# Optimization experiments

Measured on AMD Instinct MI355X. Metric: run time of the kernel, lower is better.

## Reference

```python
import jax, jax.numpy as jnp
import numpy as np

HIDDEN = 1024
HEADS = 16
HEAD_DIM = HIDDEN // HEADS


def setup_inputs() -> dict:
    key = jax.random.key(0)
    ks = jax.random.split(key, 11)
    s = 1.0 / np.sqrt(HIDDEN)
    return {
        "query": jax.random.normal(ks[0], (8, 1024, HIDDEN), dtype=jnp.float32),
        "key": jax.random.normal(ks[1], (8, 1024, HIDDEN), dtype=jnp.float32),
        "value": jax.random.normal(ks[2], (8, 1024, HIDDEN), dtype=jnp.float32),
        "Wq": jax.random.uniform(ks[3], (HIDDEN, HIDDEN), jnp.float32, -s, s),
        "bq": jax.random.uniform(ks[4], (HIDDEN,), jnp.float32, -s, s),
        "Wk": jax.random.uniform(ks[5], (HIDDEN, HIDDEN), jnp.float32, -s, s),
        "bk": jax.random.uniform(ks[6], (HIDDEN,), jnp.float32, -s, s),
        "Wv": jax.random.uniform(ks[7], (HIDDEN, HIDDEN), jnp.float32, -s, s),
        "bv": jax.random.uniform(ks[8], (HIDDEN,), jnp.float32, -s, s),
        "Wo": jax.random.uniform(ks[9], (HIDDEN, HIDDEN), jnp.float32, -s, s),
        "bo": jax.random.uniform(ks[10], (HIDDEN,), jnp.float32, -s, s),
    }


def reference(query, key, value, Wq, bq, Wk, bk, Wv, bv, Wo, bo):
    B, S, D = key.shape
    scale = jnp.sqrt(jnp.asarray(HEAD_DIM, dtype=query.dtype))
    # linear projections (torch Linear: x @ W.T + b), split into heads -> [B,H,S,hd]
    def proj(x, W, b):
        return (x @ W.T + b).reshape(B, -1, HEADS, HEAD_DIM).transpose(0, 2, 1, 3)
    q = proj(query, Wq, bq)
    k = proj(key, Wk, bk)
    v = proj(value, Wv, bv)
    # [B,H,Sq,Sk] full attention scores (module materializes them)
    energy = jnp.einsum("bhqd,bhkd->bhqk", q, k) / scale
    attention = jax.nn.softmax(energy, axis=-1)
    # dropout p=0.0 -> identity
    x = jnp.einsum("bhqk,bhkd->bhqd", attention, v)
    x = x.transpose(0, 2, 1, 3).reshape(B, -1, D)
    return x @ Wo.T + bo
```

## Files before the change

kernel.cpp:

```cpp
#include <hip/hip_runtime.h>
#include <hip/hip_bf16.h>
#include <stdint.h>

#define HIDDEN 1024
#define HEADS 16
#define HD 64
#define BATCH 8
#define SEQ 1024
#define MTOT (BATCH*SEQ)

typedef __attribute__((ext_vector_type(4))) float  f32x4;
typedef __attribute__((ext_vector_type(4))) float  float4v;
typedef __attribute__((ext_vector_type(8))) short  s16x8;
typedef __attribute__((ext_vector_type(4))) short  s16x4;
typedef __attribute__((ext_vector_type(4))) unsigned int u32x4;
typedef __bf16 bf16x8 __attribute__((ext_vector_type(8)));

#define QSCALE 0.18033688011112042f

__device__ __forceinline__ short f2bf(float f) {
  uint32_t u = __builtin_bit_cast(uint32_t, f);
  u += 0x7FFFu + ((u >> 16) & 1u);
  return (short)(u >> 16);
}
__device__ __forceinline__ bf16x8 asbf(s16x8 v) {
  return __builtin_bit_cast(bf16x8, v);
}

__device__ __forceinline__ float dpp_fmax16(float x) {
  int t;
  t = __builtin_amdgcn_update_dpp(0, __builtin_bit_cast(int, x), 0xB1, 0xF, 0xF, true);
  x = fmaxf(x, __builtin_bit_cast(float, t));
  t = __builtin_amdgcn_update_dpp(0, __builtin_bit_cast(int, x), 0x4E, 0xF, 0xF, true);
  x = fmaxf(x, __builtin_bit_cast(float, t));
  t = __builtin_amdgcn_update_dpp(0, __builtin_bit_cast(int, x), 0x141, 0xF, 0xF, true);
  x = fmaxf(x, __builtin_bit_cast(float, t));
  t = __builtin_amdgcn_update_dpp(0, __builtin_bit_cast(int, x), 0x140, 0xF, 0xF, true);
  x = fmaxf(x, __builtin_bit_cast(float, t));
  return x;
}
__device__ __forceinline__ float dpp_fadd16(float x) {
  int t;
  t = __builtin_amdgcn_update_dpp(0, __builtin_bit_cast(int, x), 0xB1, 0xF, 0xF, true);
  x += __builtin_bit_cast(float, t);
  t = __builtin_amdgcn_update_dpp(0, __builtin_bit_cast(int, x), 0x4E, 0xF, 0xF, true);
  x += __builtin_bit_cast(float, t);
  t = __builtin_amdgcn_update_dpp(0, __builtin_bit_cast(int, x), 0x141, 0xF, 0xF, true);
  x += __builtin_bit_cast(float, t);
  t = __builtin_amdgcn_update_dpp(0, __builtin_bit_cast(int, x), 0x140, 0xF, 0xF, true);
  x += __builtin_bit_cast(float, t);
  return x;
}

typedef const __attribute__((address_space(1))) void* gvp;
typedef __attribute__((address_space(3)))       void* lvp;
__device__ __forceinline__ void gl_lds16(const void* g, const void* ldsbase) {
  __builtin_amdgcn_global_load_lds((gvp)(uintptr_t)g,
                                   (lvp)(uintptr_t)(uint32_t)(uintptr_t)ldsbase,
                                   16, 0, 0);
}

__global__ __launch_bounds__(256) void cvt_x(const float* __restrict__ src,
                                             short* __restrict__ dst) {
  int i = blockIdx.x * 256 + threadIdx.x;
  float4v a = *(const float4v*)(src + (size_t)i * 8);
  float4v b = *(const float4v*)(src + (size_t)i * 8 + 4);
  s16x8 o = { f2bf(a.x), f2bf(a.y), f2bf(a.z), f2bf(a.w),
              f2bf(b.x), f2bf(b.y), f2bf(b.z), f2bf(b.w) };
  *(s16x8*)(dst + (size_t)i * 8) = o;
}

__global__ __launch_bounds__(256) void cvt_w(const float* __restrict__ s0,
                                             const float* __restrict__ s1,
                                             const float* __restrict__ s2,
                                             const float* __restrict__ s3,
                                             short* __restrict__ dst) {
  int z = blockIdx.y;
  const float* src = (z == 0) ? s0 : (z == 1) ? s1 : (z == 2) ? s2 : s3;
  int i = blockIdx.x * 256 + threadIdx.x;
  float4v a = *(const float4v*)(src + (size_t)i * 8);
  float4v b = *(const float4v*)(src + (size_t)i * 8 + 4);
  s16x8 o = { f2bf(a.x), f2bf(a.y), f2bf(a.z), f2bf(a.w),
              f2bf(b.x), f2bf(b.y), f2bf(b.z), f2bf(b.w) };
  *(s16x8*)(dst + (size_t)z * 1048576 + (size_t)i * 8) = o;
}

__global__ __launch_bounds__(256) void vtrans(const short* __restrict__ Vb,
                                              short* __restrict__ Vt) {
  __shared__ short lt[64 * 64];
  const int t = threadIdx.x;
  const int kt0 = blockIdx.x, h = blockIdx.y, b = blockIdx.z;
  const short* src = Vb + ((size_t)(b * 1024 + kt0 * 64)) * 1024 + h * 64;

  #pragma unroll
  for (int i = 0; i < 2; i++) {
    int c = t + i * 256;
    int s = c >> 3, dc = c & 7;
    s16x8 v = *(const s16x8*)(src + (size_t)s * 1024 + dc * 8);
    int dcp = dc ^ (s & 7) ^ ((s >> 3) & 7);
    *(s16x8*)(&lt[s * 64 + dcp * 8]) = v;
  }
  __syncthreads();

  short* dst = Vt + ((size_t)(b * 16 + h) * 64) * 1024 + kt0 * 64;
  #pragma unroll
  for (int i = 0; i < 2; i++) {
    int c = t + i * 256;
    int d = c >> 3, kc = c & 7;
    s16x8 o;
    #pragma unroll
    for (int j = 0; j < 8; j++) {
      int s = kc * 8 + j;
      o[j] = lt[s * 64 + (((d >> 3) ^ j ^ kc) * 8) + (d & 7)];
    }
    *(s16x8*)(dst + (size_t)d * 1024 + (kc ^ (d & 7)) * 8) = o;
  }
}

template<int CMODE>
__global__ __launch_bounds__(256, 2) void gemm_bf16_dma(
    const short* __restrict__ A, const short* __restrict__ Wb,
    const float* __restrict__ bias, void* __restrict__ Cv, float scale)
{
  __shared__ short Alds[128 * 32];
  __shared__ short Blds[128 * 32];

  const int t  = threadIdx.x;
  const int w  = t >> 6, l = t & 63, g = l >> 4, ln = l & 15;
  const int wr = w >> 1, wc = w & 1;
  const int m0 = blockIdx.x * 128, n0 = blockIdx.y * 128;

  f32x4 acc[4][4];
  #pragma unroll
  for (int i = 0; i < 4; i++)
    #pragma unroll
    for (int j = 0; j < 4; j++) acc[i][j] = (f32x4)0.0f;

  for (int k0 = 0; k0 < 1024; k0 += 32) {
    #pragma unroll
    for (int i = 0; i < 2; i++) {
      int c = i * 256 + w * 64 + l;
      int row = c >> 2, col8 = c & 3;
      gl_lds16(A  + (size_t)(m0 + row) * 1024 + k0 + col8 * 8,
               &Alds[(i * 256 + w * 64) * 8]);
      gl_lds16(Wb + (size_t)(n0 + row) * 1024 + k0 + col8 * 8,
               &Blds[(i * 256 + w * 64) * 8]);
    }
    __syncthreads();

    s16x8 af[4], bfr[4];
    #pragma unroll
    for (int mf = 0; mf < 4; mf++)
      af[mf] = *(const s16x8*)(&Alds[(wr * 64 + mf * 16 + ln) * 32 + g * 8]);
    #pragma unroll
    for (int nf = 0; nf < 4; nf++)
      bfr[nf] = *(const s16x8*)(&Blds[(wc * 64 + nf * 16 + ln) * 32 + g * 8]);

    __builtin_amdgcn_s_setprio(1);
    #pragma unroll
    for (int mf = 0; mf < 4; mf++)
      #pragma unroll
      for (int nf = 0; nf < 4; nf++)
        acc[mf][nf] = __builtin_amdgcn_mfma_f32_16x16x32_bf16(
            asbf(af[mf]), asbf(bfr[nf]), acc[mf][nf], 0, 0, 0);
    __builtin_amdgcn_s_setprio(0);
    __syncthreads();
  }

  float bv[4];
  #pragma unroll
  for (int nf = 0; nf < 4; nf++) bv[nf] = bias[n0 + wc * 64 + nf * 16 + ln];
  #pragma unroll
  for (int mf = 0; mf < 4; mf++)
    #pragma unroll
    for (int nf = 0; nf < 4; nf++)
      #pragma unroll
      for (int r = 0; r < 4; r++) {
        float vv = (acc[mf][nf][r] + bv[nf]) * scale;
        size_t idx = (size_t)(m0 + wr * 64 + mf * 16 + g * 4 + r) * 1024
                   + n0 + wc * 64 + nf * 16 + ln;
        if constexpr (CMODE == 0) ((float*)Cv)[idx] = vv;
        else if constexpr (CMODE == 1) ((short*)Cv)[idx] = f2bf(vv);
        else {
          size_t idxs = idx ^ (size_t)(((g * 4 + r) & 7) * 8);
          ((short*)Cv)[idxs] = f2bf(vv);
        }
      }
}

template<bool A_IS_BF16, bool OUT_IS_F32>
__global__ __launch_bounds__(256, 2) void gemm_bt_bias(
    const void* __restrict__ Av, const float* __restrict__ W,
    const float* __restrict__ bias, void* __restrict__ Cv, float scale)
{
  __shared__ short Alds[128 * 32];
  __shared__ short Blds[128 * 32];

  const int t  = threadIdx.x;
  const int w  = t >> 6, l = t & 63, g = l >> 4, ln = l & 15;
  const int wr = w >> 1, wc = w & 1;
  const int m0 = blockIdx.x * 128, n0 = blockIdx.y * 128;

  f32x4 acc[4][4];
  #pragma unroll
  for (int i = 0; i < 4; i++)
    #pragma unroll
    for (int j = 0; j < 4; j++) acc[i][j] = (f32x4)0.0f;

  const float* Af = (const float*)Av;
  const short* Ab = (const short*)Av;

  for (int k0 = 0; k0 < 1024; k0 += 32) {
    if constexpr (!A_IS_BF16) {
      #pragma unroll
      for (int i = 0; i < 4; i++) {
        int c = i * 256 + t;
        int row = c >> 3, c4 = c & 7;
        float4v v = *(const float4v*)(Af + (size_t)(m0 + row) * 1024 + k0 + c4 * 4);
        s16x4 p = { f2bf(v.x), f2bf(v.y), f2bf(v.z), f2bf(v.w) };
        *(s16x4*)(&Alds[row * 32 + c4 * 4]) = p;
      }
    } else {
      #pragma unroll
      for (int i = 0; i < 2; i++) {
        int c = i * 256 + t;
        int row = c >> 2, c8 = c & 3;
        *(s16x8*)(&Alds[row * 32 + c8 * 8]) =
            *(const s16x8*)(Ab + (size_t)(m0 + row) * 1024 + k0 + c8 * 8);
      }
    }
    #pragma unroll
    for (int i = 0; i < 4; i++) {
      int c = i * 256 + t;
      int row = c >> 3, c4 = c & 7;
      float4v v = *(const float4v*)(W + (size_t)(n0 + row) * 1024 + k0 + c4 * 4);
      s16x4 p = { f2bf(v.x), f2bf(v.y), f2bf(v.z), f2bf(v.w) };
      *(s16x4*)(&Blds[row * 32 + c4 * 4]) = p;
    }
    __syncthreads();

    s16x8 af[4], bfr[4];
    #pragma unroll
    for (int mf = 0; mf < 4; mf++)
      af[mf] = *(const s16x8*)(&Alds[(wr * 64 + mf * 16 + ln) * 32 + g * 8]);
    #pragma unroll
    for (int nf = 0; nf < 4; nf++)
      bfr[nf] = *(const s16x8*)(&Blds[(wc * 64 + nf * 16 + ln) * 32 + g * 8]);

    #pragma unroll
    for (int mf = 0; mf < 4; mf++)
      #pragma unroll
      for (int nf = 0; nf < 4; nf++)
        acc[mf][nf] = __builtin_amdgcn_mfma_f32_16x16x32_bf16(
            asbf(af[mf]), asbf(bfr[nf]), acc[mf][nf], 0, 0, 0);
    __syncthreads();
  }

  float bv[4];
  #pragma unroll
  for (int nf = 0; nf < 4; nf++) bv[nf] = bias[n0 + wc * 64 + nf * 16 + ln];
  #pragma unroll
  for (int mf = 0; mf < 4; mf++)
    #pragma unroll
    for (int nf = 0; nf < 4; nf++)
      #pragma unroll
      for (int r = 0; r < 4; r++) {
        float vv = (acc[mf][nf][r] + bv[nf]) * scale;
        size_t idx = (size_t)(m0 + wr * 64 + mf * 16 + g * 4 + r) * 1024
                   + n0 + wc * 64 + nf * 16 + ln;
        if constexpr (OUT_IS_F32) ((float*)Cv)[idx] = vv;
        else                      ((short*)Cv)[idx] = f2bf(vv);
      }
}

__global__ __launch_bounds__(256, 2) void flash_attn(
    const short* __restrict__ Q, const short* __restrict__ Kswz,
    const short* __restrict__ Vt, short* __restrict__ CTX)
{
  __shared__ short Klds[2][64 * 64];
  __shared__ short Vlds[2][64 * 64];

  const int t  = threadIdx.x;
  const int w  = t >> 6, l = t & 63, g = l >> 4, ln = l & 15;
  const int rb0 = g & 1, rb1 = g >> 1;
  const bool sendK = (rb0 ^ rb1) != 0;
  const int bh   = blockIdx.x & 127;
  const int tile = blockIdx.x >> 7;
  const int b = bh >> 4, h = bh & 15;
  const size_t rowbase = (size_t)b * SEQ;
  const int colbase = h * HD;
  const int q0w = tile * 128 + w * 32;

  const short* Kg = Kswz + rowbase * 1024 + colbase;
  const short* Vg = Vt + (size_t)bh * 65536;
  const int c0 = w * 64 + l;

  s16x8 qf[2][2];
  #pragma unroll
  for (int mf = 0; mf < 2; mf++)
    #pragma unroll
    for (int kf = 0; kf < 2; kf++)
      qf[mf][kf] = *(const s16x8*)(Q + (rowbase + q0w + mf * 16 + ln) * 1024
                                     + colbase + kf * 32 + g * 8);

  f32x4 acc_o[2][4];
  #pragma unroll
  for (int i = 0; i < 2; i++)
    #pragma unroll
    for (int j = 0; j < 4; j++) acc_o[i][j] = (f32x4)0.0f;

  float m_run[2] = { -1e30f, -1e30f };
  float l_run[2] = { 0.0f, 0.0f };

  auto STAGE = [&](int buf, int nt) {
    #pragma unroll
    for (int i = 0; i < 2; i++) {
      int c = c0 + i * 256;
      gl_lds16(Kg + (size_t)(nt * 64 + (c >> 3)) * 1024 + (c & 7) * 8,
               &Klds[buf][(i * 256 + w * 64) * 8]);
      gl_lds16(Vg + (size_t)(c >> 3) * 1024 + nt * 64 + (c & 7) * 8,
               &Vlds[buf][(i * 256 + w * 64) * 8]);
    }
  };

  STAGE(0, 0);
  __syncthreads();

  int cur = 0;
  for (int kt = 0; kt < 16; kt++) {
    if (kt < 15) STAGE(cur ^ 1, kt + 1);

    const short* Kc = &Klds[cur][0];
    const short* Vc = &Vlds[cur][0];

    f32x4 sT[4][2];
    #pragma unroll
    for (int i = 0; i < 4; i++)
      #pragma unroll
      for (int j = 0; j < 2; j++) sT[i][j] = (f32x4)0.0f;

    __builtin_amdgcn_s_setprio(1);
    #pragma unroll
    for (int kf = 0; kf < 2; kf++) {
      s16x8 kfr[4];
      #pragma unroll
      for (int nf = 0; nf < 4; nf++)
        kfr[nf] = *(const s16x8*)(Kc + (nf * 16 + ln) * 64
                                     + (((kf * 4 + g) ^ (ln & 7)) * 8));
      #pragma unroll
      for (int kk4 = 0; kk4 < 4; kk4++)
        #pragma unroll
        for (int kq = 0; kq < 2; kq++)
          sT[kk4][kq] = __builtin_amdgcn_mfma_f32_16x16x32_bf16(
              asbf(kfr[kk4]), asbf(qf[kq][kf]), sT[kk4][kq], 0, 0, 0);
    }
    __builtin_amdgcn_s_setprio(0);

    float rm[2];
    #pragma unroll
    for (int kq = 0; kq < 2; kq++) {
      float mx = sT[0][kq][0];
      #pragma unroll
      for (int kk4 = 0; kk4 < 4; kk4++)
        #pragma unroll
        for (int r = 0; r < 4; r++)
          if (kk4 | r) mx = fmaxf(mx, sT[kk4][kq][r]);
      mx = fmaxf(mx, __shfl_xor(mx, 16));
      mx = fmaxf(mx, __shfl_xor(mx, 32));
      rm[kq] = mx;
    }
    float worst = fmaxf(rm[0] - m_run[0], rm[1] - m_run[1]);

    if (__all(worst <= 8.0f)) {
      #pragma unroll
      for (int kq = 0; kq < 2; kq++) {
        float m0v = m_run[kq];
        float rs = 0.0f;
        #pragma unroll
        for (int kk4 = 0; kk4 < 4; kk4++)
          #pragma unroll
          for (int r = 0; r < 4; r++) {
            float pv = exp2f(sT[kk4][kq][r] - m0v);
            sT[kk4][kq][r] = pv;
            rs += pv;
          }
        l_run[kq] += rs;
      }
    } else {
      float sc[2];
      #pragma unroll
      for (int kq = 0; kq < 2; kq++) {
        float mnew = fmaxf(m_run[kq], rm[kq]);
        sc[kq] = exp2f(m_run[kq] - mnew);
        m_run[kq] = mnew;
        float rs = 0.0f;
        #pragma unroll
        for (int kk4 = 0; kk4 < 4; kk4++)
          #pragma unroll
          for (int r = 0; r < 4; r++) {
            float pv = exp2f(sT[kk4][kq][r] - mnew);
            sT[kk4][kq][r] = pv;
            rs += pv;
          }
        l_run[kq] = l_run[kq] * sc[kq] + rs;
      }
      #pragma unroll
      for (int mf = 0; mf < 2; mf++)
        #pragma unroll
        for (int r = 0; r < 4; r++) {
          float scr = __shfl(sc[mf], g * 4 + r);
          #pragma unroll
          for (int nf = 0; nf < 4; nf++) acc_o[mf][nf][r] *= scr;
        }
    }

    uint32_t D[4][2][2];
    #pragma unroll
    for (int kk4 = 0; kk4 < 4; kk4++)
      #pragma unroll
      for (int kq = 0; kq < 2; kq++) {
        asm("v_cvt_pk_bf16_f32 %0, %1, %2"
            : "=v"(D[kk4][kq][0]) : "v"(sT[kk4][kq][0]), "v"(sT[kk4][kq][1]));
        asm("v_cvt_pk_bf16_f32 %0, %1, %2"
            : "=v"(D[kk4][kq][1]) : "v"(sT[kk4][kq][2]), "v"(sT[kk4][kq][3]));
      }

    s16x8 pa[2][2];
    #pragma unroll
    for (int kq = 0; kq < 2; kq++)
      #pragma unroll
      for (int kp = 0; kp < 2; kp++) {
        uint32_t K0 = rb1 ? D[2*kp+1][kq][0] : D[2*kp][kq][0];
        uint32_t K1 = rb1 ? D[2*kp+1][kq][1] : D[2*kp][kq][1];
        uint32_t S0 = rb1 ? D[2*kp][kq][0]   : D[2*kp+1][kq][0];
        uint32_t S1 = rb1 ? D[2*kp][kq][1]   : D[2*kp+1][kq][1];
        uint32_t R0 = (uint32_t)__shfl_xor((int)S0, 32);
        uint32_t R1 = (uint32_t)__shfl_xor((int)S1, 32);
        uint32_t T0 = sendK ? K0 : R0, T1 = sendK ? K1 : R1;
        uint32_t V0 = sendK ? R0 : K0, V1 = sendK ? R1 : K1;
        uint32_t U0 = (uint32_t)__shfl_xor((int)T0, 16);
        uint32_t U1 = (uint32_t)__shfl_xor((int)T1, 16);
        u32x4 dw = { rb0 ? U0 : V0, rb0 ? U1 : V1,
                     rb0 ? V0 : U0, rb0 ? V1 : U1 };
        pa[kq][kp] = __builtin_bit_cast(s16x8, dw);
      }

    s16x8 vbf[4][2];
    #pragma unroll
    for (int nf = 0; nf < 4; nf++)
      #pragma unroll
      for (int kf = 0; kf < 2; kf++)
        vbf[nf][kf] = *(const s16x8*)(Vc + (nf * 16 + ln) * 64
                                         + (((kf * 4 + g) ^ (ln & 7)) * 8));

    __builtin_amdgcn_s_setprio(1);
    #pragma unroll
    for (int kf = 0; kf < 2; kf++)
      #pragma unroll
      for (int mf = 0; mf < 2; mf++)
        #pragma unroll
        for (int nf = 0; nf < 4; nf++)
          acc_o[mf][nf] = __builtin_amdgcn_mfma_f32_16x16x32_bf16(
              asbf(pa[mf][kf]), asbf(vbf[nf][kf]), acc_o[mf][nf], 0, 0, 0);
    __builtin_amdgcn_s_setprio(0);

    __syncthreads();
    cur ^= 1;
  }

  #pragma unroll
  for (int kq = 0; kq < 2; kq++) {
    l_run[kq] += __shfl_xor(l_run[kq], 16);
    l_run[kq] += __shfl_xor(l_run[kq], 32);
  }
  #pragma unroll
  for (int mf = 0; mf < 2; mf++)
    #pragma unroll
    for (int r = 0; r < 4; r++) {
      float inv = 1.0f / __shfl(l_run[mf], g * 4 + r);
      size_t row = rowbase + q0w + mf * 16 + g * 4 + r;
      #pragma unroll
      for (int nf = 0; nf < 4; nf++)
        CTX[row * 1024 + colbase + nf * 16 + ln] = f2bf(acc_o[mf][nf][r] * inv);
    }
}

__global__ __launch_bounds__(256, 2) void flash_attn_fb(
    const short* __restrict__ Q, const short* __restrict__ K,
    const short* __restrict__ V, short* __restrict__ CTX)
{
  __shared__ short Klds[2][64 * 64];
  __shared__ short Vtl [2][64 * 64];
  __shared__ short Plds[4][32 * 72];

  const int t  = threadIdx.x;
  const int w  = t >> 6, l = t & 63, g = l >> 4, ln = l & 15;
  const int tile = blockIdx.x & 7;
  const int bh   = blockIdx.x >> 3;
  const int b = bh >> 4, h = bh & 15;
  const size_t rowbase = (size_t)b * SEQ;
  const int colbase = h * HD;
  const int q0w = tile * 128 + w * 32;

  const int kk0  = t >> 3;
  const int dblk = t & 7;
  const int ksw  = (dblk ^ (kk0 & 7)) * 8;
  const int kWr  = kk0 * 64 + dblk * 8;
  const short* Kg = K + rowbase * 1024 + colbase + ksw;
  const short* Vg = V + rowbase * 1024 + colbase + dblk * 8;

  s16x8 qf[2][2];
  #pragma unroll
  for (int mf = 0; mf < 2; mf++)
    #pragma unroll
    for (int kf = 0; kf < 2; kf++)
      qf[mf][kf] = *(const s16x8*)(Q + (rowbase + q0w + mf * 16 + ln) * 1024
                                     + colbase + kf * 32 + g * 8);

  f32x4 acc_o[2][4];
  #pragma unroll
  for (int i = 0; i < 2; i++)
    #pragma unroll
    for (int j = 0; j < 4; j++) acc_o[i][j] = (f32x4)0.0f;

  float m_run[2][4], l_run[2][4];
  #pragma unroll
  for (int i = 0; i < 2; i++)
    #pragma unroll
    for (int r = 0; r < 4; r++) { m_run[i][r] = -1e30f; l_run[i][r] = 0.0f; }

  auto storeKV = [&](int buf, s16x8 ka, s16x8 kb, s16x8 va, s16x8 vb8) {
    short* Kd = &Klds[buf][0];
    short* Vd = &Vtl[buf][0];
    *(s16x8*)(Kd + kWr)        = ka;
    *(s16x8*)(Kd + kWr + 2048) = kb;
    #pragma unroll
    for (int e = 0; e < 8; e++) {
      int a0 = (dblk * 8 + e) * 64 + (kk0 ^ ((e ^ dblk) * 8));
      Vd[a0]      = va[e];
      Vd[a0 ^ 32] = vb8[e];
    }
  };

  s16x8 kvA = *(const s16x8*)(Kg + (size_t)kk0 * 1024);
  s16x8 kvB = *(const s16x8*)(Kg + (size_t)(kk0 + 32) * 1024);
  s16x8 vvA = *(const s16x8*)(Vg + (size_t)kk0 * 1024);
  s16x8 vvB = *(const s16x8*)(Vg + (size_t)(kk0 + 32) * 1024);
  storeKV(0, kvA, kvB, vvA, vvB);

  int cur = 0;
  for (int kt = 0; kt < 16; kt++) {
    if (kt < 15) {
      const size_t r0 = (size_t)((kt + 1) * 64 + kk0) * 1024;
      kvA = *(const s16x8*)(Kg + r0);
      kvB = *(const s16x8*)(Kg + r0 + 32 * 1024);
      vvA = *(const s16x8*)(Vg + r0);
      vvB = *(const s16x8*)(Vg + r0 + 32 * 1024);
    }
    __syncthreads();

    const short* Kc = &Klds[cur][0];
    const short* Vc = &Vtl[cur][0];

    f32x4 s_acc[2][4];
    #pragma unroll
    for (int i = 0; i < 2; i++)
      #pragma unroll
      for (int j = 0; j < 4; j++) s_acc[i][j] = (f32x4)0.0f;

    #pragma unroll
    for (int kf = 0; kf < 2; kf++) {
      s16x8 kfr[4];
      #pragma unroll
      for (int nf = 0; nf < 4; nf++)
        kfr[nf] = *(const s16x8*)(Kc + (nf * 16 + ln) * 64
                                     + (((kf * 4 + g) ^ (ln & 7)) * 8));
      #pragma unroll
      for (int mf = 0; mf < 2; mf++)
        #pragma unroll
        for (int nf = 0; nf < 4; nf++)
          s_acc[mf][nf] = __builtin_amdgcn_mfma_f32_16x16x32_bf16(
              asbf(qf[mf][kf]), asbf(kfr[nf]), s_acc[mf][nf], 0, 0, 0);
    }

    float smax[2][4];
    float worst = -1e30f;
    #pragma unroll
    for (int mf = 0; mf < 2; mf++)
      #pragma unroll
      for (int r = 0; r < 4; r++) {
        float mx = fmaxf(fmaxf(s_acc[mf][0][r], s_acc[mf][1][r]),
                         fmaxf(s_acc[mf][2][r], s_acc[mf][3][r]));
        mx = dpp_fmax16(mx);
        smax[mf][r] = mx;
        worst = fmaxf(worst, mx - m_run[mf][r]);
      }

    if (__all(worst <= 8.0f)) {
      #pragma unroll
      for (int mf = 0; mf < 2; mf++)
        #pragma unroll
        for (int r = 0; r < 4; r++) {
          float m0v = m_run[mf][r];
          float rs = 0.0f;
          #pragma unroll
          for (int nf = 0; nf < 4; nf++) {
            float pv = exp2f(s_acc[mf][nf][r] - m0v);
            s_acc[mf][nf][r] = pv;
            rs += pv;
          }
          l_run[mf][r] += rs;
        }
    } else {
      #pragma unroll
      for (int mf = 0; mf < 2; mf++)
        #pragma unroll
        for (int r = 0; r < 4; r++) {
          float mnew = fmaxf(m_run[mf][r], smax[mf][r]);
          float sc = exp2f(m_run[mf][r] - mnew);
          m_run[mf][r] = mnew;
          float rs = 0.0f;
          #pragma unroll
          for (int nf = 0; nf < 4; nf++) {
            float pv = exp2f(s_acc[mf][nf][r] - mnew);
            s_acc[mf][nf][r] = pv;
            rs += pv;
          }
          l_run[mf][r] = l_run[mf][r] * sc + rs;
          #pragma unroll
          for (int nf = 0; nf < 4; nf++) acc_o[mf][nf][r] *= sc;
        }
    }

    short* Pw = &Plds[w][0];
    #pragma unroll
    for (int mf = 0; mf < 2; mf++)
      #pragma unroll
      for (int nf = 0; nf < 4; nf++) {
        uint32_t p01, p23;
        asm("v_cvt_pk_bf16_f32 %0, %1, %2"
            : "=v"(p01) : "v"(s_acc[mf][nf][0]), "v"(s_acc[mf][nf][1]));
        asm("v_cvt_pk_bf16_f32 %0, %1, %2"
            : "=v"(p23) : "v"(s_acc[mf][nf][2]), "v"(s_acc[mf][nf][3]));
        int pb = (mf * 16 + g * 4) * 72 + ((nf * 16 + ln) ^ (g << 3));
        Pw[pb]       = (short)p01;
        Pw[pb + 72]  = (short)(p01 >> 16);
        Pw[pb + 144] = (short)p23;
        Pw[pb + 216] = (short)(p23 >> 16);
      }

    s16x8 pa[2][2], vbf[4][2];
    #pragma unroll
    for (int mf = 0; mf < 2; mf++)
      #pragma unroll
      for (int kf = 0; kf < 2; kf++)
        pa[mf][kf] = *(const s16x8*)(
            &Pw[(mf * 16 + ln) * 72 + (((kf * 4 + g) ^ (ln >> 2)) << 3)]);
    #pragma unroll
    for (int nf = 0; nf < 4; nf++)
      #pragma unroll
      for (int kf = 0; kf < 2; kf++) {
        int d  = nf * 16 + ln;
        int sw = (d & 7) ^ (d >> 3);
        vbf[nf][kf] = *(const s16x8*)(Vc + d * 64 + ((kf * 32 + g * 8) ^ (sw * 8)));
      }

    #pragma unroll
    for (int kf = 0; kf < 2; kf++)
      #pragma unroll
      for (int mf = 0; mf < 2; mf++)
        #pragma unroll
        for (int nf = 0; nf < 4; nf++)
          acc_o[mf][nf] = __builtin_amdgcn_mfma_f32_16x16x32_bf16(
              asbf(pa[mf][kf]), asbf(vbf[nf][kf]), acc_o[mf][nf], 0, 0, 0);

    if (kt < 15) {
      storeKV(cur ^ 1, kvA, kvB, vvA, vvB);
      cur ^= 1;
    }
  }

  #pragma unroll
  for (int mf = 0; mf < 2; mf++)
    #pragma unroll
    for (int r = 0; r < 4; r++) {
      float inv = 1.0f / dpp_fadd16(l_run[mf][r]);
      size_t row = rowbase + q0w + mf * 16 + g * 4 + r;
      #pragma unroll
      for (int nf = 0; nf < 4; nf++)
        CTX[row * 1024 + colbase + nf * 16 + ln] = f2bf(acc_o[mf][nf][r] * inv);
    }
}

extern "C" void kernel_launch(void* const* d_in, const int* in_sizes, int n_in,
                              void* d_out, int out_size, void* d_ws, size_t ws_size,
                              hipStream_t stream) {
  const float* query = (const float*)d_in[0];
  const float* key   = (const float*)d_in[1];
  const float* value = (const float*)d_in[2];
  const float* Wq = (const float*)d_in[3];
  const float* bq = (const float*)d_in[4];
  const float* Wk = (const float*)d_in[5];
  const float* bk = (const float*)d_in[6];
  const float* Wv = (const float*)d_in[7];
  const float* bv = (const float*)d_in[8];
  const float* Wo = (const float*)d_in[9];
  const float* bo = (const float*)d_in[10];

  const size_t E = (size_t)MTOT * 1024;
  short* Qb = (short*)d_ws;
  short* Kb = Qb + E;
  short* Vb = Kb + E;
  short* Cx = Vb + E;
  short* T  = Cx + E;
  short* Wb = T  + E;

  const size_t need = (5 * E + 4ull * 1048576) * 2;
  dim3 gg(MTOT / 128, HIDDEN / 128), bb(256);
  dim3 fg(BATCH * HEADS * (SEQ / 128));

  if (ws_size >= need) {
    cvt_w<<<dim3(512, 4), bb, 0, stream>>>(Wq, Wk, Wv, Wo, Wb);
    cvt_x<<<4096, bb, 0, stream>>>(query, T);
    gemm_bf16_dma<1><<<gg, bb, 0, stream>>>(T, Wb + 0 * 1048576, bq, Qb, QSCALE);
    cvt_x<<<4096, bb, 0, stream>>>(key, T);
    gemm_bf16_dma<2><<<gg, bb, 0, stream>>>(T, Wb + 1 * 1048576, bk, Kb, 1.0f);
    cvt_x<<<4096, bb, 0, stream>>>(value, T);
    gemm_bf16_dma<1><<<gg, bb, 0, stream>>>(T, Wb + 2 * 1048576, bv, Vb, 1.0f);
    vtrans<<<dim3(16, 16, 8), bb, 0, stream>>>(Vb, T);
    flash_attn<<<fg, bb, 0, stream>>>(Qb, Kb, T, Cx);
    gemm_bf16_dma<0><<<gg, bb, 0, stream>>>(Cx, Wb + 3 * 1048576, bo, (float*)d_out, 1.0f);
  } else {
    gemm_bt_bias<false, false><<<gg, bb, 0, stream>>>(query, Wq, bq, Qb, QSCALE);
    gemm_bt_bias<false, false><<<gg, bb, 0, stream>>>(key,   Wk, bk, Kb, 1.0f);
    gemm_bt_bias<false, false><<<gg, bb, 0, stream>>>(value, Wv, bv, Vb, 1.0f);
    flash_attn_fb<<<fg, bb, 0, stream>>>(Qb, Kb, Vb, Cx);
    gemm_bt_bias<true, true><<<gg, bb, 0, stream>>>(Cx, Wo, bo, (float*)d_out, 1.0f);
  }
}
```

Measured before the change: 224.6 us.

## Load K and V fragments directly from global memory in flash attention

The attention kernel no longer stages K and V tiles into double-buffered LDS with async global-to-LDS copies and barriers. Each wave now reads its MFMA operand fragments straight from global memory, using unswizzled K and V layouts, and the K projection and V transpose drop their swizzled output. This removes the LDS traffic and per-tile __syncthreads, but each wave fetches the same K/V data separately through the cache. It also gives up the prefetch overlap the double buffer provided, so global load latency is exposed inside the loop.

```diff
diff --git a/kernel.cpp b/kernel.cpp
--- a/kernel.cpp
+++ b/kernel.cpp
@@ -113,7 +113,7 @@
       int s = kc * 8 + j;
       o[j] = lt[s * 64 + (((d >> 3) ^ j ^ kc) * 8) + (d & 7)];
     }
-    *(s16x8*)(dst + (size_t)d * 1024 + (kc ^ (d & 7)) * 8) = o;
+    *(s16x8*)(dst + (size_t)d * 1024 + kc * 8) = o;
   }
 }
 
@@ -274,12 +274,9 @@
 }
 
 __global__ __launch_bounds__(256, 2) void flash_attn(
-    const short* __restrict__ Q, const short* __restrict__ Kswz,
+    const short* __restrict__ Kb, const short* __restrict__ Q,
     const short* __restrict__ Vt, short* __restrict__ CTX)
 {
-  __shared__ short Klds[2][64 * 64];
-  __shared__ short Vlds[2][64 * 64];
-
   const int t  = threadIdx.x;
   const int w  = t >> 6, l = t & 63, g = l >> 4, ln = l & 15;
   const int rb0 = g & 1, rb1 = g >> 1;
@@ -291,9 +288,8 @@
   const int colbase = h * HD;
   const int q0w = tile * 128 + w * 32;
 
-  const short* Kg = Kswz + rowbase * 1024 + colbase;
-  const short* Vg = Vt + (size_t)bh * 65536;
-  const int c0 = w * 64 + l;
+  const short* Kl = Kb + (rowbase + ln) * 1024 + colbase;
+  const short* Vl = Vt + ((size_t)bh * 64 + ln) * 1024;
 
   s16x8 qf[2][2];
   #pragma unroll
@@ -312,26 +308,16 @@
   float m_run[2] = { -1e30f, -1e30f };
   float l_run[2] = { 0.0f, 0.0f };
 
-  auto STAGE = [&](int buf, int nt) {
-    #pragma unroll
-    for (int i = 0; i < 2; i++) {
-      int c = c0 + i * 256;
-      gl_lds16(Kg + (size_t)(nt * 64 + (c >> 3)) * 1024 + (c & 7) * 8,
-               &Klds[buf][(i * 256 + w * 64) * 8]);
-      gl_lds16(Vg + (size_t)(c >> 3) * 1024 + nt * 64 + (c & 7) * 8,
-               &Vlds[buf][(i * 256 + w * 64) * 8]);
-    }
-  };
-
-  STAGE(0, 0);
-  __syncthreads();
-
-  int cur = 0;
   for (int kt = 0; kt < 16; kt++) {
-    if (kt < 15) STAGE(cur ^ 1, kt + 1);
-
-    const short* Kc = &Klds[cur][0];
-    const short* Vc = &Vlds[cur][0];
+    const int k0 = kt * 64;
+
+    s16x8 kA[2][4];
+    #pragma unroll
+    for (int kf = 0; kf < 2; kf++)
+      #pragma unroll
+      for (int nf = 0; nf < 4; nf++)
+        kA[kf][nf] = *(const s16x8*)(Kl + (size_t)(k0 + nf * 16) * 1024
+                                        + kf * 32 + g * 8);
 
     f32x4 sT[4][2];
     #pragma unroll
@@ -341,20 +327,22 @@
 
     __builtin_amdgcn_s_setprio(1);
     #pragma unroll
-    for (int kf = 0; kf < 2; kf++) {
-      s16x8 kfr[4];
-      #pragma unroll
-      for (int nf = 0; nf < 4; nf++)
-        kfr[nf] = *(const s16x8*)(Kc + (nf * 16 + ln) * 64
-                                     + (((kf * 4 + g) ^ (ln & 7)) * 8));
+    for (int kf = 0; kf < 2; kf++)
       #pragma unroll
       for (int kk4 = 0; kk4 < 4; kk4++)
         #pragma unroll
         for (int kq = 0; kq < 2; kq++)
           sT[kk4][kq] = __builtin_amdgcn_mfma_f32_16x16x32_bf16(
-              asbf(kfr[kk4]), asbf(qf[kq][kf]), sT[kk4][kq], 0, 0, 0);
-    }
+              asbf(kA[kf][kk4]), asbf(qf[kq][kf]), sT[kk4][kq], 0, 0, 0);
     __builtin_amdgcn_s_setprio(0);
+
+    s16x8 vbf[4][2];
+    #pragma unroll
+    for (int nf = 0; nf < 4; nf++)
+      #pragma unroll
+      for (int kf = 0; kf < 2; kf++)
+        vbf[nf][kf] = *(const s16x8*)(Vl + (size_t)(nf * 16) * 1024
+                                         + k0 + kf * 32 + g * 8);
 
     float rm[2];
     #pragma unroll
@@ -445,14 +433,6 @@
         pa[kq][kp] = __builtin_bit_cast(s16x8, dw);
       }
 
-    s16x8 vbf[4][2];
-    #pragma unroll
-    for (int nf = 0; nf < 4; nf++)
-      #pragma unroll
-      for (int kf = 0; kf < 2; kf++)
-        vbf[nf][kf] = *(const s16x8*)(Vc + (nf * 16 + ln) * 64
-                                         + (((kf * 4 + g) ^ (ln & 7)) * 8));
-
     __builtin_amdgcn_s_setprio(1);
     #pragma unroll
     for (int kf = 0; kf < 2; kf++)
@@ -463,9 +443,6 @@
           acc_o[mf][nf] = __builtin_amdgcn_mfma_f32_16x16x32_bf16(
               asbf(pa[mf][kf]), asbf(vbf[nf][kf]), acc_o[mf][nf], 0, 0, 0);
     __builtin_amdgcn_s_setprio(0);
-
-    __syncthreads();
-    cur ^= 1;
   }
 
   #pragma unroll
@@ -724,11 +701,11 @@
     cvt_x<<<4096, bb, 0, stream>>>(query, T);
     gemm_bf16_dma<1><<<gg, bb, 0, stream>>>(T, Wb + 0 * 1048576, bq, Qb, QSCALE);
     cvt_x<<<4096, bb, 0, stream>>>(key, T);
-    gemm_bf16_dma<2><<<gg, bb, 0, stream>>>(T, Wb + 1 * 1048576, bk, Kb, 1.0f);
+    gemm_bf16_dma<1><<<gg, bb, 0, stream>>>(T, Wb + 1 * 1048576, bk, Kb, 1.0f);
     cvt_x<<<4096, bb, 0, stream>>>(value, T);
     gemm_bf16_dma<1><<<gg, bb, 0, stream>>>(T, Wb + 2 * 1048576, bv, Vb, 1.0f);
     vtrans<<<dim3(16, 16, 8), bb, 0, stream>>>(Vb, T);
-    flash_attn<<<fg, bb, 0, stream>>>(Qb, Kb, T, Cx);
+    flash_attn<<<fg, bb, 0, stream>>>(Kb, Qb, T, Cx);
     gemm_bf16_dma<0><<<gg, bb, 0, stream>>>(Cx, Wb + 3 * 1048576, bo, (float*)d_out, 1.0f);
   } else {
     gemm_bt_bias<false, false><<<gg, bb, 0, stream>>>(query, Wq, bq, Qb, QSCALE);
```

After: 264.4 us. +17.7%, slower.
